# Optimization experiments

Measured on AMD Instinct MI355X. Metric: run time of the kernel, lower is better.

## Reference

```python
import math
import jax, jax.numpy as jnp
import numpy as np

N_HEAD = 16

def skew(QEr):
    # QEr: (B, H, L, L) where last dim indexes relative positions via Er_t
    B, H, L, _ = QEr.shape
    padded = jnp.pad(QEr, ((0, 0), (0, 0), (0, 0), (1, 0)))        # (B,H,L,L+1)
    reshaped = padded.reshape(B, H, L + 1, L)                       # (B,H,L+1,L)
    return reshaped[:, :, 1:, :]                                    # (B,H,L,L)

def setup_inputs() -> dict:
    key = jax.random.key(0)
    ks = jax.random.split(key, 6)
    B, L, D = 2, 2048, 1024
    hs = D // N_HEAD
    block_size = 2048
    return {
        "x": jax.random.normal(ks[0], (B, L, D), dtype=jnp.float32),
        "W_attn": jax.random.normal(ks[1], (D, 3 * D), dtype=jnp.float32) * 0.02,
        "b_attn": jnp.zeros((3 * D,), dtype=jnp.float32),
        "W_proj": jax.random.normal(ks[2], (D, D), dtype=jnp.float32) * 0.02,
        "b_proj": jnp.zeros((D,), dtype=jnp.float32),
        "Er": jax.random.normal(ks[3], (block_size, hs), dtype=jnp.float32),
    }

def reference(x, W_attn, b_attn, W_proj, b_proj, Er):
    B, L, D = x.shape
    H = N_HEAD
    hs = D // H
    qkv = x @ W_attn + b_attn                                       # (B,L,3D)
    q, k, v = jnp.split(qkv, 3, axis=-1)
    q = q.reshape(B, L, H, hs).transpose(0, 2, 1, 3)                # (B,H,L,hs)
    k = k.reshape(B, L, H, hs).transpose(0, 2, 1, 3)
    v = v.reshape(B, L, H, hs).transpose(0, 2, 1, 3)
    start = Er.shape[0] - L
    Er_t = Er[start:, :].T                                          # (hs,L)
    QEr = jnp.einsum('bhld,de->bhle', q, Er_t)                      # (B,H,L,L)
    Srel = skew(QEr)
    QK_t = jnp.einsum('bhqd,bhkd->bhqk', q, k)
    scale = 1.0 / math.sqrt(hs)
    att = (QK_t + Srel) * scale
    causal = jnp.tril(jnp.ones((L, L), dtype=bool))
    att = jnp.where(causal[None, None, :, :], att, -jnp.inf)
    att = jax.nn.softmax(att, axis=-1)
    y = jnp.einsum('bhqk,bhkd->bhqd', att, v)                       # (B,H,L,hs)
    y = y.transpose(0, 2, 1, 3).reshape(B, L, D)
    return y @ W_proj + b_proj
```

## Files before the change

kernel.cpp:

```cpp
#include <hip/hip_runtime.h>
#include <stdint.h>

#define L_SEQ 2048
#define D_MODEL 1024
#define NHEAD 16
#define HS 64
#define B_BATCH 2
#define QSCALE 0.1803368801111243f

typedef __bf16 bf16x8 __attribute__((ext_vector_type(8)));
typedef float f32x4 __attribute__((ext_vector_type(4)));

__device__ __forceinline__ float fexp2(float x) {
  return __builtin_amdgcn_exp2f(x);
}

__device__ __forceinline__ unsigned short f2b(float f) {
  unsigned int u = __float_as_uint(f);
  u += 0x7fffu + ((u >> 16) & 1u);
  return (unsigned short)(u >> 16);
}
__device__ __forceinline__ unsigned int pk2(float a, float b) {
  return (unsigned int)f2b(a) | ((unsigned int)f2b(b) << 16);
}
__device__ __forceinline__ unsigned int cvtpk(float a, float b) {
  unsigned int r;
  asm("v_cvt_pk_bf16_f32 %0, %1, %2" : "=v"(r) : "v"(a), "v"(b));
  return r;
}

union U8 { uint4 v; unsigned short s[8]; };

__device__ __forceinline__ void ldsload16(const unsigned short* g, unsigned short* l) {
  __builtin_amdgcn_global_load_lds(
      (const __attribute__((address_space(1))) unsigned int*)g,
      (__attribute__((address_space(3))) unsigned int*)l, 16, 0, 0);
}

__device__ __forceinline__ bf16x8 frag_ld(const unsigned short* base, int row, int ks, int quad) {
  const int unit = (ks * 4 + quad) ^ (row & 7);
  return *(const bf16x8*)(base + row * 64 + unit * 8);
}

__global__ __launch_bounds__(256) void prep(
    const float* __restrict__ x, const float* __restrict__ Wa,
    const float* __restrict__ Wp, const float* __restrict__ Er,
    unsigned short* __restrict__ xb, unsigned short* __restrict__ wabT,
    unsigned short* __restrict__ wpbT, unsigned short* __restrict__ erb) {
  __shared__ unsigned short tt[64][65];
  int gb = blockIdx.x;
  if (gb < 2048) {
    int i = gb * 256 + threadIdx.x;
    const float4* s4 = (const float4*)x;
    float4 a = s4[i * 2], b = s4[i * 2 + 1];
    U8 u;
    u.s[0] = f2b(a.x); u.s[1] = f2b(a.y); u.s[2] = f2b(a.z); u.s[3] = f2b(a.w);
    u.s[4] = f2b(b.x); u.s[5] = f2b(b.y); u.s[6] = f2b(b.z); u.s[7] = f2b(b.w);
    ((uint4*)xb)[i] = u.v;
    return;
  }
  gb -= 2048;
  if (gb < 68) {
    int i = gb * 256 + threadIdx.x;
    if (i < 16384) {
      const float4* s4 = (const float4*)Er;
      float4 a = s4[i * 2], b = s4[i * 2 + 1];
      U8 u;
      u.s[0] = f2b(a.x); u.s[1] = f2b(a.y); u.s[2] = f2b(a.z); u.s[3] = f2b(a.w);
      u.s[4] = f2b(b.x); u.s[5] = f2b(b.y); u.s[6] = f2b(b.z); u.s[7] = f2b(b.w);
      ((uint4*)erb)[i] = u.v;
    } else {
      ((uint4*)erb)[i] = make_uint4(0u, 0u, 0u, 0u);
    }
    return;
  }
  gb -= 68;
  const float* src;
  unsigned short* dst;
  int N, nbx;
  if (gb < 768) { src = Wa; dst = wabT; N = 3072; nbx = 48; }
  else { gb -= 768; src = Wp; dst = wpbT; N = 1024; nbx = 16; }
  const int n0 = (gb % nbx) * 64, k0 = (gb / nbx) * 64;
  const int c = threadIdx.x & 63, r0 = threadIdx.x >> 6;
#pragma unroll
  for (int i = 0; i < 16; i++) {
    int r = r0 * 16 + i;
    tt[r][c] = f2b(src[(size_t)(k0 + r) * N + n0 + c]);
  }
  __syncthreads();
  const int n = threadIdx.x >> 2, ks = (threadIdx.x & 3) * 16;
  U8 u0, u1;
#pragma unroll
  for (int j = 0; j < 8; j++) {
    u0.s[j] = tt[ks + j][n];
    u1.s[j] = tt[ks + 8 + j][n];
  }
  unsigned short* d = dst + (size_t)(n0 + n) * 1024 + k0 + ks;
  *(uint4*)d = u0.v;
  *(uint4*)(d + 8) = u1.v;
}

__global__ __launch_bounds__(256, 3) void gemm_qkv(
    const unsigned short* __restrict__ A, const unsigned short* __restrict__ Bt,
    const float* __restrict__ bias, unsigned short* __restrict__ qbuf,
    unsigned short* __restrict__ kbuf, unsigned short* __restrict__ vbufT,
    int M, int N, int K) {
  __shared__ unsigned short As[128 * 64];
  __shared__ unsigned short Bs[128 * 64];
  const int tid = threadIdx.x, lane = tid & 63, w = tid >> 6;
  const int wm = w >> 1, wn = w & 1, quad = lane >> 4, lc = lane & 15;
  const int bm = blockIdx.y, bn = blockIdx.x;
  const int l8 = lane >> 3, u8 = ((lane & 7) ^ l8) * 8;
  const unsigned short* Ab = A + (size_t)bm * 128 * K;
  const unsigned short* Bb = Bt + (size_t)bn * 128 * K;

  f32x4 z4 = {0.f, 0.f, 0.f, 0.f};
  f32x4 acc[4][4];
#pragma unroll
  for (int mb = 0; mb < 4; mb++)
#pragma unroll
    for (int nb = 0; nb < 4; nb++) acc[mb][nb] = z4;

  for (int kk = 0; kk < K; kk += 64) {
    if (kk) __syncthreads();
#pragma unroll
    for (int i = 0; i < 4; i++) {
      int ch = w * 4 + i;
      ldsload16(Ab + (size_t)(ch * 8 + l8) * K + kk + u8, &As[ch * 512]);
      ldsload16(Bb + (size_t)(ch * 8 + l8) * K + kk + u8, &Bs[ch * 512]);
    }
    __syncthreads();
#pragma unroll
    for (int ks = 0; ks < 2; ks++) {
      bf16x8 af[4], bfv[4];
#pragma unroll
      for (int mb = 0; mb < 4; mb++) af[mb] = frag_ld(As, wm * 64 + mb * 16 + lc, ks, quad);
#pragma unroll
      for (int nb = 0; nb < 4; nb++) bfv[nb] = frag_ld(Bs, wn * 64 + nb * 16 + lc, ks, quad);
#pragma unroll
      for (int mb = 0; mb < 4; mb++)
#pragma unroll
        for (int nb = 0; nb < 4; nb++)
          acc[mb][nb] = __builtin_amdgcn_mfma_f32_16x16x32_bf16(af[mb], bfv[nb],
                                                               acc[mb][nb], 0, 0, 0);
    }
  }

#pragma unroll
  for (int nb = 0; nb < 4; nb++) {
    const int n = bn * 128 + wn * 64 + nb * 16 + lc;
    const float bv = bias[n];
    const int which = n >> 10;
    const int rem = n & 1023;
    const int h = rem >> 6, d = rem & 63;
#pragma unroll
    for (int mb = 0; mb < 4; mb++) {
      const int m0 = bm * 128 + wm * 64 + mb * 16 + quad * 4;
      const int b = m0 >> 11, l0 = m0 & 2047;
      if (which == 2) {
        float v0 = acc[mb][nb][0] + bv, v1 = acc[mb][nb][1] + bv;
        float v2 = acc[mb][nb][2] + bv, v3 = acc[mb][nb][3] + bv;
        uint2 pv;
        pv.x = pk2(v0, v1);
        pv.y = pk2(v2, v3);
        *(uint2*)&vbufT[((size_t)(b * NHEAD + h) * HS + d) * L_SEQ + l0] = pv;
      } else {
        const float sc = which == 0 ? QSCALE : 1.0f;
        unsigned short* dst = (which == 0) ? qbuf : kbuf;
#pragma unroll
        for (int reg = 0; reg < 4; reg++) {
          float val = (acc[mb][nb][reg] + bv) * sc;
          dst[((size_t)(b * NHEAD + h) * L_SEQ + l0 + reg) * HS + d] = f2b(val);
        }
      }
    }
  }
}

__global__ __launch_bounds__(256, 2) void gemm_proj(
    const unsigned short* __restrict__ A, const unsigned short* __restrict__ Bt,
    const float* __restrict__ bias, float* __restrict__ out, int M, int N, int K) {
  __shared__ unsigned short As[128 * 64];
  __shared__ unsigned short Bs[64 * 64];
  const int tid = threadIdx.x, lane = tid & 63, w = tid >> 6;
  const int quad = lane >> 4, lc = lane & 15;
  const int bm = blockIdx.y, bn = blockIdx.x;
  const int l8 = lane >> 3, u8 = ((lane & 7) ^ l8) * 8;
  const unsigned short* Ab = A + (size_t)bm * 128 * K;
  const unsigned short* Bb = Bt + (size_t)bn * 64 * K;

  f32x4 z4 = {0.f, 0.f, 0.f, 0.f};
  f32x4 acc[2][4];
#pragma unroll
  for (int mb = 0; mb < 2; mb++)
#pragma unroll
    for (int nb = 0; nb < 4; nb++) acc[mb][nb] = z4;

  for (int kk = 0; kk < K; kk += 64) {
    if (kk) __syncthreads();
#pragma unroll
    for (int i = 0; i < 4; i++) {
      int ch = w * 4 + i;
      ldsload16(Ab + (size_t)(ch * 8 + l8) * K + kk + u8, &As[ch * 512]);
    }
#pragma unroll
    for (int i = 0; i < 2; i++) {
      int ch = w * 2 + i;
      ldsload16(Bb + (size_t)(ch * 8 + l8) * K + kk + u8, &Bs[ch * 512]);
    }
    __syncthreads();
#pragma unroll
    for (int ks = 0; ks < 2; ks++) {
      bf16x8 af[2], bfv[4];
#pragma unroll
      for (int mb = 0; mb < 2; mb++) af[mb] = frag_ld(As, w * 32 + mb * 16 + lc, ks, quad);
#pragma unroll
      for (int nb = 0; nb < 4; nb++) bfv[nb] = frag_ld(Bs, nb * 16 + lc, ks, quad);
#pragma unroll
      for (int mb = 0; mb < 2; mb++)
#pragma unroll
        for (int nb = 0; nb < 4; nb++)
          acc[mb][nb] = __builtin_amdgcn_mfma_f32_16x16x32_bf16(af[mb], bfv[nb],
                                                               acc[mb][nb], 0, 0, 0);
    }
  }

#pragma unroll
  for (int nb = 0; nb < 4; nb++) {
    const int n = bn * 64 + nb * 16 + lc;
    const float bv = bias[n];
#pragma unroll
    for (int mb = 0; mb < 2; mb++) {
#pragma unroll
      for (int reg = 0; reg < 4; reg++) {
        const int m = bm * 128 + w * 32 + mb * 16 + quad * 4 + reg;
        out[(size_t)m * N + n] = acc[mb][nb][reg] + bv;
      }
    }
  }
}

__global__ __launch_bounds__(256, 4) void flash_attn_rel(
    const unsigned short* __restrict__ qb, const unsigned short* __restrict__ kb,
    const unsigned short* __restrict__ vbT, const unsigned short* __restrict__ erb,
    unsigned short* __restrict__ yb) {
  __shared__ unsigned short Ks[64 * 64];
  __shared__ unsigned short Vt[64 * 64];
  __shared__ float Twf[4][1344];

  const int tid = threadIdx.x, lane = tid & 63, w = tid >> 6;
  const int quad = lane >> 4, lc = lane & 15;
  const int bh = blockIdx.x;
  const int b = bh >> 4, h = bh & 15;
  const int y = (int)blockIdx.y;
  int qt;
  if (y < 8) qt = 31 - y;
  else if (y < 16) qt = y - 8;
  else if (y < 24) qt = 39 - y;
  else qt = y - 16;
  const int q0 = qt * 64;
  const int qg0 = q0 + w * 16;
  const size_t hoff = (size_t)bh * L_SEQ * HS;
  float* TwfW = Twf[w];
  unsigned short* TwpW = (unsigned short*)TwfW;
  const int l8 = lane >> 3, u8 = ((lane & 7) ^ l8) * 8;
  const f32x4 z4 = {0.f, 0.f, 0.f, 0.f};

  bf16x8 qf[2];
  {
    const unsigned short* qrow = qb + hoff + (size_t)(qg0 + lc) * HS;
    qf[0] = *(const bf16x8*)(qrow + quad * 8);
    qf[1] = *(const bf16x8*)(qrow + 32 + quad * 8);
  }
  f32x4 Oacc[4];
#pragma unroll
  for (int db = 0; db < 4; db++) Oacc[db] = z4;
  float psum_acc = 0.0f;

  const unsigned short* kgb = kb + hoff;
  const unsigned short* vgbT = vbT + (size_t)bh * HS * L_SEQ;
  const unsigned short* erow0 =
      erb + (size_t)((L_SEQ - 64) - q0 + 48 - 16 * w + lc) * HS + quad * 8;

  for (int k0 = 0; k0 <= q0; k0 += 64) {
    __syncthreads();
#pragma unroll
    for (int i = 0; i < 2; i++) {
      int ch = w * 2 + i;
      ldsload16(kgb + (size_t)(k0 + ch * 8 + l8) * HS + u8, &Ks[ch * 512]);
      ldsload16(vgbT + (size_t)(ch * 8 + l8) * L_SEQ + k0 + u8, &Vt[ch * 512]);
    }
    const unsigned short* erow = erow0 + (size_t)k0 * HS;
    bf16x8 ef[2][5];
#pragma unroll
    for (int ks = 0; ks < 2; ks++)
#pragma unroll
      for (int eb = 0; eb < 5; eb++)
        ef[ks][eb] = *(const bf16x8*)(erow + eb * (16 * HS) + ks * 32);
    __syncthreads();

    f32x4 sacc[4], tacc[5];
#pragma unroll
    for (int i = 0; i < 4; i++) sacc[i] = z4;
#pragma unroll
    for (int i = 0; i < 5; i++) tacc[i] = z4;
#pragma unroll
    for (int ks = 0; ks < 2; ks++) {
#pragma unroll
      for (int kbi = 0; kbi < 4; kbi++) {
        bf16x8 a = frag_ld(Ks, kbi * 16 + lc, ks, quad);
        sacc[kbi] = __builtin_amdgcn_mfma_f32_16x16x32_bf16(a, qf[ks], sacc[kbi], 0, 0, 0);
      }
#pragma unroll
      for (int eb = 0; eb < 5; eb++)
        tacc[eb] = __builtin_amdgcn_mfma_f32_16x16x32_bf16(ef[ks][eb], qf[ks], tacc[eb], 0, 0, 0);
    }
#pragma unroll
    for (int eb = 0; eb < 5; eb++)
      *(f32x4*)&TwfW[lc * 84 + eb * 16 + quad * 4] = tacc[eb];
    asm volatile("" ::: "memory");

    float p[4][4], ps = 0.0f;
    const int tbase = lc * 84 + (15 - lc);
    if (k0 == q0) {
      const int qrow = w * 16 + lc;
#pragma unroll
      for (int kbi = 0; kbi < 4; kbi++)
#pragma unroll
        for (int reg = 0; reg < 4; reg++) {
          const int kk = kbi * 16 + quad * 4 + reg;
          float t = TwfW[tbase + kk];
          float v = (kk > qrow) ? -1e30f : (sacc[kbi][reg] + t);
          p[kbi][reg] = fexp2(v);
          ps += p[kbi][reg];
        }
    } else {
#pragma unroll
      for (int kbi = 0; kbi < 4; kbi++)
#pragma unroll
        for (int reg = 0; reg < 4; reg++) {
          float t = TwfW[tbase + kbi * 16 + quad * 4 + reg];
          p[kbi][reg] = fexp2(sacc[kbi][reg] + t);
          ps += p[kbi][reg];
        }
    }
    psum_acc += ps;
#pragma unroll
    for (int kbi = 0; kbi < 4; kbi++) {
      uint2 pk;
      pk.x = cvtpk(p[kbi][0], p[kbi][1]);
      pk.y = cvtpk(p[kbi][2], p[kbi][3]);
      const int k = kbi * 16 + quad * 4;
      *(uint2*)&TwpW[lc * 64 + (((k >> 3) ^ (lc & 7)) << 3) + (k & 7)] = pk;
    }
    asm volatile("" ::: "memory");

#pragma unroll
    for (int ks = 0; ks < 2; ks++) {
      bf16x8 pf = frag_ld(TwpW, lc, ks, quad);
#pragma unroll
      for (int db = 0; db < 4; db++) {
        bf16x8 av = frag_ld(Vt, db * 16 + lc, ks, quad);
        Oacc[db] = __builtin_amdgcn_mfma_f32_16x16x32_bf16(av, pf, Oacc[db], 0, 0, 0);
      }
    }
  }

  psum_acc += __shfl_xor(psum_acc, 16, 64);
  psum_acc += __shfl_xor(psum_acc, 32, 64);
  const float inv = 1.0f / psum_acc;

  __syncthreads();
  unsigned short* Yt = (unsigned short*)&Twf[0][0];
#pragma unroll
  for (int db = 0; db < 4; db++) {
    uint2 pk;
    pk.x = cvtpk(Oacc[db][0] * inv, Oacc[db][1] * inv);
    pk.y = cvtpk(Oacc[db][2] * inv, Oacc[db][3] * inv);
    *(uint2*)&Yt[(w * 16 + lc) * 72 + db * 16 + quad * 4] = pk;
  }
  __syncthreads();
  {
    const int r = tid >> 2, seg = (tid & 3) * 16;
    uint4 a0 = *(const uint4*)&Yt[r * 72 + seg];
    uint4 a1 = *(const uint4*)&Yt[r * 72 + seg + 8];
    unsigned short* d = yb + (size_t)((size_t)b * L_SEQ + q0 + r) * D_MODEL + h * HS + seg;
    *(uint4*)d = a0;
    *(uint4*)(d + 8) = a1;
  }
}

extern "C" void kernel_launch(void* const* d_in, const int* in_sizes, int n_in,
                              void* d_out, int out_size, void* d_ws, size_t ws_size,
                              hipStream_t stream) {
  const float* x = (const float*)d_in[0];
  const float* W_attn = (const float*)d_in[1];
  const float* b_attn = (const float*)d_in[2];
  const float* W_proj = (const float*)d_in[3];
  const float* b_proj = (const float*)d_in[4];
  const float* Er = (const float*)d_in[5];
  float* out = (float*)d_out;

  const int n_x = B_BATCH * L_SEQ * D_MODEL;
  const int n_wa = D_MODEL * 3 * D_MODEL;
  const int n_wp = D_MODEL * D_MODEL;
  const int n_er_pad = (L_SEQ + 128) * HS;
  const int n_head = B_BATCH * NHEAD * L_SEQ * HS;

  unsigned short* xb = (unsigned short*)d_ws;
  unsigned short* wabT = xb + n_x;
  unsigned short* wpbT = wabT + n_wa;
  unsigned short* erb = wpbT + n_wp;
  unsigned short* qbuf = erb + n_er_pad;
  unsigned short* kbuf = qbuf + n_head;
  unsigned short* vbufT = kbuf + n_head;
  unsigned short* ybuf = vbufT + n_head;

  prep<<<3140, 256, 0, stream>>>(x, W_attn, W_proj, Er, xb, wabT, wpbT, erb);

  gemm_qkv<<<dim3(24, 32), 256, 0, stream>>>(xb, wabT, b_attn, qbuf, kbuf, vbufT,
                                             B_BATCH * L_SEQ, 3 * D_MODEL, D_MODEL);

  flash_attn_rel<<<dim3(B_BATCH * NHEAD, 32), 256, 0, stream>>>(qbuf, kbuf, vbufT,
                                                                erb, ybuf);

  gemm_proj<<<dim3(16, 32), 256, 0, stream>>>(ybuf, wpbT, b_proj, out,
                                              B_BATCH * L_SEQ, D_MODEL, D_MODEL);
}
```

Baseline: 227.7 us.

## Remap workgroups per XCD for L2 locality and stage Er tiles in LDS

All three kernels now use a 1D grid with a remapping that puts workgroups sharing the same weight or head columns on the same XCD (wgid & 7), so they share that XCD's L2. The attention kernel also loads the relative-position Er tile for each K block into shared memory with async loads, instead of every wave fetching its own fragments from global memory into registers. The attention work order changes from an interleaved long/short ordering to strictly longest-first, and launch bounds drop from 4 to 3 blocks per CU because of the extra LDS. Risks are lower occupancy in attention and worse load balance from the new tile order.

After: 193.4 us. 1.18x faster.

```diff
diff --git a/kernel.cpp b/kernel.cpp
--- a/kernel.cpp
+++ b/kernel.cpp
@@ -109,7 +109,10 @@
   __shared__ unsigned short Bs[128 * 64];
   const int tid = threadIdx.x, lane = tid & 63, w = tid >> 6;
   const int wm = w >> 1, wn = w & 1, quad = lane >> 4, lc = lane & 15;
-  const int bm = blockIdx.y, bn = blockIdx.x;
+  const int wgid = blockIdx.x;
+  const int xcd = wgid & 7, t = wgid >> 3;
+  const int bnr = t % 3, bm = t / 3;
+  const int bn = xcd * 3 + bnr;
   const int l8 = lane >> 3, u8 = ((lane & 7) ^ l8) * 8;
   const unsigned short* Ab = A + (size_t)bm * 128 * K;
   const unsigned short* Bb = Bt + (size_t)bn * 128 * K;
@@ -184,7 +187,10 @@
   __shared__ unsigned short Bs[64 * 64];
   const int tid = threadIdx.x, lane = tid & 63, w = tid >> 6;
   const int quad = lane >> 4, lc = lane & 15;
-  const int bm = blockIdx.y, bn = blockIdx.x;
+  const int wgid = blockIdx.x;
+  const int xcd = wgid & 7, t = wgid >> 3;
+  const int bnr = t & 1, bm = t >> 1;
+  const int bn = xcd * 2 + bnr;
   const int l8 = lane >> 3, u8 = ((lane & 7) ^ l8) * 8;
   const unsigned short* Ab = A + (size_t)bm * 128 * K;
   const unsigned short* Bb = Bt + (size_t)bn * 64 * K;
@@ -240,24 +246,23 @@
   }
 }
 
-__global__ __launch_bounds__(256, 4) void flash_attn_rel(
+__global__ __launch_bounds__(256, 3) void flash_attn_rel(
     const unsigned short* __restrict__ qb, const unsigned short* __restrict__ kb,
     const unsigned short* __restrict__ vbT, const unsigned short* __restrict__ erb,
     unsigned short* __restrict__ yb) {
   __shared__ unsigned short Ks[64 * 64];
   __shared__ unsigned short Vt[64 * 64];
-  __shared__ float Twf[4][1344];
+  __shared__ unsigned short Es[128 * 64];
+  __shared__ float Twf[4][16 * 84];
 
   const int tid = threadIdx.x, lane = tid & 63, w = tid >> 6;
   const int quad = lane >> 4, lc = lane & 15;
-  const int bh = blockIdx.x;
+  const int wgid = blockIdx.x;
+  const int xcd = wgid & 7, r7 = wgid >> 3;
+  const int bhr = r7 & 3, y = r7 >> 2;
+  const int bh = xcd * 4 + bhr;
   const int b = bh >> 4, h = bh & 15;
-  const int y = (int)blockIdx.y;
-  int qt;
-  if (y < 8) qt = 31 - y;
-  else if (y < 16) qt = y - 8;
-  else if (y < 24) qt = 39 - y;
-  else qt = y - 16;
+  const int qt = 31 - y;
   const int q0 = qt * 64;
   const int qg0 = q0 + w * 16;
   const size_t hoff = (size_t)bh * L_SEQ * HS;
@@ -279,8 +284,7 @@
 
   const unsigned short* kgb = kb + hoff;
   const unsigned short* vgbT = vbT + (size_t)bh * HS * L_SEQ;
-  const unsigned short* erow0 =
-      erb + (size_t)((L_SEQ - 64) - q0 + 48 - 16 * w + lc) * HS + quad * 8;
+  const int ebw = 48 - w * 16;
 
   for (int k0 = 0; k0 <= q0; k0 += 64) {
     __syncthreads();
@@ -290,13 +294,12 @@
       ldsload16(kgb + (size_t)(k0 + ch * 8 + l8) * HS + u8, &Ks[ch * 512]);
       ldsload16(vgbT + (size_t)(ch * 8 + l8) * L_SEQ + k0 + u8, &Vt[ch * 512]);
     }
-    const unsigned short* erow = erow0 + (size_t)k0 * HS;
-    bf16x8 ef[2][5];
-#pragma unroll
-    for (int ks = 0; ks < 2; ks++)
-#pragma unroll
-      for (int eb = 0; eb < 5; eb++)
-        ef[ks][eb] = *(const bf16x8*)(erow + eb * (16 * HS) + ks * 32);
+    const int e0 = (L_SEQ - 64) - q0 + k0;
+#pragma unroll
+    for (int i = 0; i < 4; i++) {
+      int ch = w * 4 + i;
+      ldsload16(erb + (size_t)(e0 + ch * 8 + l8) * HS + u8, &Es[ch * 512]);
+    }
     __syncthreads();
 
     f32x4 sacc[4], tacc[5];
@@ -312,8 +315,10 @@
         sacc[kbi] = __builtin_amdgcn_mfma_f32_16x16x32_bf16(a, qf[ks], sacc[kbi], 0, 0, 0);
       }
 #pragma unroll
-      for (int eb = 0; eb < 5; eb++)
-        tacc[eb] = __builtin_amdgcn_mfma_f32_16x16x32_bf16(ef[ks][eb], qf[ks], tacc[eb], 0, 0, 0);
+      for (int eb = 0; eb < 5; eb++) {
+        bf16x8 a = frag_ld(Es, ebw + eb * 16 + lc, ks, quad);
+        tacc[eb] = __builtin_amdgcn_mfma_f32_16x16x32_bf16(a, qf[ks], tacc[eb], 0, 0, 0);
+      }
     }
 #pragma unroll
     for (int eb = 0; eb < 5; eb++)
@@ -371,7 +376,7 @@
   const float inv = 1.0f / psum_acc;
 
   __syncthreads();
-  unsigned short* Yt = (unsigned short*)&Twf[0][0];
+  unsigned short* Yt = Es;
 #pragma unroll
   for (int db = 0; db < 4; db++) {
     uint2 pk;
@@ -418,12 +423,11 @@
 
   prep<<<3140, 256, 0, stream>>>(x, W_attn, W_proj, Er, xb, wabT, wpbT, erb);
 
-  gemm_qkv<<<dim3(24, 32), 256, 0, stream>>>(xb, wabT, b_attn, qbuf, kbuf, vbufT,
-                                             B_BATCH * L_SEQ, 3 * D_MODEL, D_MODEL);
-
-  flash_attn_rel<<<dim3(B_BATCH * NHEAD, 32), 256, 0, stream>>>(qbuf, kbuf, vbufT,
-                                                                erb, ybuf);
-
-  gemm_proj<<<dim3(16, 32), 256, 0, stream>>>(ybuf, wpbT, b_proj, out,
-                                              B_BATCH * L_SEQ, D_MODEL, D_MODEL);
-}
+  gemm_qkv<<<768, 256, 0, stream>>>(xb, wabT, b_attn, qbuf, kbuf, vbufT,
+                                    B_BATCH * L_SEQ, 3 * D_MODEL, D_MODEL);
+
+  flash_attn_rel<<<1024, 256, 0, stream>>>(qbuf, kbuf, vbufT, erb, ybuf);
+
+  gemm_proj<<<512, 256, 0, stream>>>(ybuf, wpbT, b_proj, out,
+                                     B_BATCH * L_SEQ, D_MODEL, D_MODEL);
+}
```
